# Performance work log

Measured on AMD Instinct MI355X. Metric: run time of the kernel, lower is better.

The kernel has to match this reference:

```python
import jax, jax.numpy as jnp
import numpy as np
import math

B, T, C = 2, 2048, 2048
N_HEAD = 16
N_KV = 4
GROUP = N_HEAD // N_KV
HS = C // N_HEAD
WINDOW = 1024
SINK = 4


def setup_inputs() -> dict:
    key = jax.random.key(0)
    ks = jax.random.split(key, 5)
    s = 1.0 / math.sqrt(C)
    return {
        "x": jax.random.normal(ks[0], (B, T, C), dtype=jnp.float32),
        "Wq": jax.random.normal(ks[1], (C, C), dtype=jnp.float32) * s,
        "Wk": jax.random.normal(ks[2], (N_KV * HS, C), dtype=jnp.float32) * s,
        "Wv": jax.random.normal(ks[3], (N_KV * HS, C), dtype=jnp.float32) * s,
        "Wo": jax.random.normal(ks[4], (C, C), dtype=jnp.float32) * s,
    }


def _sliding_window_sink_mask(t):
    i = jnp.arange(t)[:, None]  # query index
    j = jnp.arange(t)[None, :]  # key index
    causal = j <= i
    band = j >= i - (WINDOW - 1)
    mask = causal & band
    mask = mask | (j < SINK)          # sink columns always visible
    mask = mask & ((i >= SINK) | causal)  # sink rows stay strictly causal
    return mask  # (T, T) bool


def reference(x, Wq, Wk, Wv, Wo):
    b, t, c = x.shape
    q = (x @ Wq.T).reshape(b, t, N_HEAD, HS).transpose(0, 2, 1, 3)
    # group q heads by kv head: (B, n_kv, group, T, hs)
    q = q.reshape(b, N_KV, GROUP, t, HS)
    k = (x @ Wk.T).reshape(b, t, N_KV, HS).transpose(0, 2, 1, 3)  # (B, n_kv, T, hs)
    v = (x @ Wv.T).reshape(b, t, N_KV, HS).transpose(0, 2, 1, 3)
    scale = 1.0 / math.sqrt(HS)
    # scores over full TxT (faithful to original, K/V expansion done via broadcast)
    att = jnp.einsum('bkgqd,bkjd->bkgqj', q, k) * scale
    mask = _sliding_window_sink_mask(t)  # (T, T)
    att = jnp.where(mask[None, None, None, :, :], att, -jnp.inf)
    att = jax.nn.softmax(att, axis=-1)
    y = jnp.einsum('bkgqj,bkjd->bkgqd', att, v)
    y = y.reshape(b, N_HEAD, t, HS).transpose(0, 2, 1, 3).reshape(b, t, c)
    return y @ Wo.T
```

## Files before the change

### kernel.cpp

```cpp
#include <hip/hip_runtime.h>


#define T_SEQ 2048
#define NKV   4
#define HS    128
#define CDIM  2048
#define QKVN  3072
#define WIN   1024
#define SINKN 4
#define PSTR  68

typedef __bf16 bf16x8 __attribute__((ext_vector_type(8)));
typedef float  f32x4  __attribute__((ext_vector_type(4)));

#define MFMA16(A, B, C) __builtin_amdgcn_mfma_f32_16x16x32_bf16(A, B, C, 0, 0, 0)
#define EXP2(x) __builtin_amdgcn_exp2f(x)

__device__ inline unsigned short f2bu(float f) {
  unsigned int u = __float_as_uint(f);
  u += 0x7fffu + ((u >> 16) & 1u);
  return (unsigned short)(u >> 16);
}
__device__ inline unsigned int pkhi(float f0, float f1) {
  return __builtin_amdgcn_perm(__float_as_uint(f1), __float_as_uint(f0),
                               0x07060302u);
}
__device__ inline __bf16 us2b(unsigned short u) {
  union { unsigned short u; __bf16 b; } t; t.u = u; return t.b;
}
__device__ inline f32x4 fzero4() { f32x4 z = {0.f, 0.f, 0.f, 0.f}; return z; }

__device__ __forceinline__ void glds16(const void* g, const void* lds_uniform) {
  typedef __attribute__((address_space(1))) void gv;
  typedef __attribute__((address_space(3))) void lv;
  __builtin_amdgcn_global_load_lds((gv*)(unsigned long long)g,
                                   (lv*)(unsigned int)(unsigned long long)lds_uniform,
                                   16, 0, 0);
}

#define SZ_X  8388608
#define SZ_WQ 4194304
#define SZ_WK 1048576
#define OFF_WQ (SZ_X)
#define OFF_WK (SZ_X + SZ_WQ)
#define OFF_WV (OFF_WK + SZ_WK)
#define OFF_WO (OFF_WV + SZ_WK)
#define SZ_ALL (OFF_WO + SZ_WQ)

__global__ __launch_bounds__(256) void f2b_all(const float* __restrict__ x,
                                               const float* __restrict__ wq,
                                               const float* __restrict__ wk,
                                               const float* __restrict__ wv,
                                               const float* __restrict__ wo,
                                               unsigned short* __restrict__ out,
                                               float qs) {
  int i = (blockIdx.x * 256 + threadIdx.x) * 4;
  const float* src; int off; float sc = 1.0f;
  if (i < OFF_WQ)      { src = x;  off = 0; }
  else if (i < OFF_WK) { src = wq; off = OFF_WQ; sc = qs; }
  else if (i < OFF_WV) { src = wk; off = OFF_WK; }
  else if (i < OFF_WO) { src = wv; off = OFF_WV; }
  else                 { src = wo; off = OFF_WO; }
  float4 v = *reinterpret_cast<const float4*>(src + (i - off));
  ushort4 o;
  o.x = f2bu(v.x * sc); o.y = f2bu(v.y * sc);
  o.z = f2bu(v.z * sc); o.w = f2bu(v.w * sc);
  *reinterpret_cast<ushort4*>(out + i) = o;
}

__device__ inline void storeC(unsigned short* p, float v) { *p = f2bu(v); }
__device__ inline void storeC(float* p, float v) { *p = v; }

template <typename OutT>
__global__ __launch_bounds__(512, 2) void gemm256(const unsigned short* __restrict__ A,
                                                  const unsigned short* __restrict__ B,
                                                  OutT* __restrict__ C,
                                                  int M, int N, int K) {
  __shared__ __align__(16) unsigned short As[2][16384];
  __shared__ __align__(16) unsigned short Bs[2][16384];
  const int tid  = threadIdx.x;
  const int wave = tid >> 6, lane = tid & 63;
  const int quad = lane >> 4, l16 = lane & 15;
  const int wmi  = wave >> 2, wni = wave & 3;
  const int sx   = ((l16 >> 3) & 1) << 5;

  const int tmn  = M >> 8;
  const int qq   = gridDim.x >> 3;
  const int swzb = (blockIdx.x & 7) * qq + (blockIdx.x >> 3);
  const int tm   = (swzb % tmn) << 8;
  const int tn   = (swzb / tmn) << 8;

  const int logl = (lane * 16) ^ (((lane >> 5) & 1) << 5);
  const int srow = logl >> 6;
  const int scol = (logl & 63) >> 1;
  const int NT   = K >> 6;

  auto issueA = [&](int tt, int ch) {
    glds16(&A[(size_t)(tm + (ch & 15) * 16 + srow) * K + (tt << 6) + (ch >> 4) * 32 + scol],
           (const char*)As + ((tt & 1) << 15) + ch * 1024);
  };
  auto issueB = [&](int tt, int ch) {
    glds16(&B[(size_t)(tn + (ch & 15) * 16 + srow) * K + (tt << 6) + (ch >> 4) * 32 + scol],
           (const char*)Bs + ((tt & 1) << 15) + ch * 1024);
  };

  f32x4 acc[8][4];
#pragma unroll
  for (int i = 0; i < 8; ++i)
#pragma unroll
    for (int j = 0; j < 4; ++j) acc[i][j] = fzero4();

  issueB(0, wave); issueB(0, 8 + wave); issueB(0, 16 + wave); issueB(0, 24 + wave);
  issueA(0, wave); issueA(0, 16 + wave); issueA(0, 8 + wave); issueA(0, 24 + wave);
  if (NT > 1) {
    issueB(1, wave); issueB(1, 8 + wave);
    asm volatile("s_waitcnt vmcnt(2)" ::: "memory");
  } else {
    asm volatile("s_waitcnt vmcnt(0)" ::: "memory");
  }
  __builtin_amdgcn_s_barrier();

#pragma unroll 2
  for (int t = 0; t < NT; ++t) {
    const char* Asc = (const char*)As + ((t & 1) << 15);
    const char* Bsc = (const char*)Bs + ((t & 1) << 15);
    const bool h1 = (t + 1 < NT), h2 = (t + 2 < NT);
    bf16x8 aq[4], bq[4];

#pragma unroll
    for (int g = 0; g < 4; ++g)
      bq[g] = *reinterpret_cast<const bf16x8*>(
          Bsc + (((wni * 64 + g * 16 + l16) << 6) + ((quad * 16) ^ sx)));
#pragma unroll
    for (int f = 0; f < 4; ++f)
      aq[f] = *reinterpret_cast<const bf16x8*>(
          Asc + (((wmi * 128 + f * 16 + l16) << 6) + ((quad * 16) ^ sx)));
    if (h1) { issueB(t + 1, 16 + wave); issueB(t + 1, 24 + wave); }
    __builtin_amdgcn_s_barrier();
    asm volatile("s_waitcnt lgkmcnt(0)" ::: "memory");
    __builtin_amdgcn_s_setprio(1);
#pragma unroll
    for (int f = 0; f < 4; ++f)
#pragma unroll
      for (int g = 0; g < 4; ++g) acc[f][g] = MFMA16(aq[f], bq[g], acc[f][g]);
    __builtin_amdgcn_s_setprio(0);
    __builtin_amdgcn_s_barrier();

#pragma unroll
    for (int f = 0; f < 4; ++f)
      aq[f] = *reinterpret_cast<const bf16x8*>(
          Asc + (((wmi * 128 + 64 + f * 16 + l16) << 6) + ((quad * 16) ^ sx)));
    if (h1) { issueA(t + 1, wave); issueA(t + 1, 16 + wave); }
    __builtin_amdgcn_s_barrier();
    asm volatile("s_waitcnt lgkmcnt(0)" ::: "memory");
    __builtin_amdgcn_s_setprio(1);
#pragma unroll
    for (int f = 0; f < 4; ++f)
#pragma unroll
      for (int g = 0; g < 4; ++g) acc[4 + f][g] = MFMA16(aq[f], bq[g], acc[4 + f][g]);
    __builtin_amdgcn_s_setprio(0);
    __builtin_amdgcn_s_barrier();

#pragma unroll
    for (int g = 0; g < 4; ++g)
      bq[g] = *reinterpret_cast<const bf16x8*>(
          Bsc + (16384 + ((wni * 64 + g * 16 + l16) << 6) + ((quad * 16) ^ sx)));
#pragma unroll
    for (int f = 0; f < 4; ++f)
      aq[f] = *reinterpret_cast<const bf16x8*>(
          Asc + (16384 + ((wmi * 128 + f * 16 + l16) << 6) + ((quad * 16) ^ sx)));
    if (h1) { issueA(t + 1, 8 + wave); issueA(t + 1, 24 + wave); }
    __builtin_amdgcn_s_barrier();
    asm volatile("s_waitcnt lgkmcnt(0)" ::: "memory");
    __builtin_amdgcn_s_setprio(1);
#pragma unroll
    for (int f = 0; f < 4; ++f)
#pragma unroll
      for (int g = 0; g < 4; ++g) acc[f][g] = MFMA16(aq[f], bq[g], acc[f][g]);
    __builtin_amdgcn_s_setprio(0);
    __builtin_amdgcn_s_barrier();

#pragma unroll
    for (int f = 0; f < 4; ++f)
      aq[f] = *reinterpret_cast<const bf16x8*>(
          Asc + (16384 + ((wmi * 128 + 64 + f * 16 + l16) << 6) + ((quad * 16) ^ sx)));
    if (h2) { issueB(t + 2, wave); issueB(t + 2, 8 + wave); }
    __builtin_amdgcn_s_barrier();
    asm volatile("s_waitcnt lgkmcnt(0)" ::: "memory");
    __builtin_amdgcn_s_setprio(1);
#pragma unroll
    for (int f = 0; f < 4; ++f)
#pragma unroll
      for (int g = 0; g < 4; ++g) acc[4 + f][g] = MFMA16(aq[f], bq[g], acc[4 + f][g]);
    __builtin_amdgcn_s_setprio(0);
    if (h2) asm volatile("s_waitcnt vmcnt(2)" ::: "memory");
    else    asm volatile("s_waitcnt vmcnt(0)" ::: "memory");
    __builtin_amdgcn_s_barrier();
  }

#pragma unroll
  for (int fi = 0; fi < 8; ++fi)
#pragma unroll
    for (int g = 0; g < 4; ++g)
#pragma unroll
      for (int r = 0; r < 4; ++r) {
        const int row = tm + wmi * 128 + fi * 16 + quad * 4 + r;
        const int col = tn + wni * 64 + g * 16 + l16;
        storeC(&C[(size_t)row * N + col], acc[fi][g][r]);
      }
}

template <typename OutT>
__global__ __launch_bounds__(512, 2) void gemm_bn128(const unsigned short* __restrict__ A,
                                                     const unsigned short* __restrict__ B,
                                                     OutT* __restrict__ C,
                                                     int M, int N, int K) {
  __shared__ __align__(16) unsigned short As[2][16384];
  __shared__ __align__(16) unsigned short Bs[2][8192];
  const int tid  = threadIdx.x;
  const int wave = tid >> 6, lane = tid & 63;
  const int quad = lane >> 4, l16 = lane & 15;
  const int wmi  = wave >> 1, wni = wave & 1;
  const int sx   = ((l16 >> 3) & 1) << 5;

  const int tmn  = M >> 8;
  const int qq   = gridDim.x >> 3;
  const int swzb = (blockIdx.x & 7) * qq + (blockIdx.x >> 3);
  const int tm   = (swzb % tmn) << 8;
  const int tn   = (swzb / tmn) << 7;

  const int logl = (lane * 16) ^ (((lane >> 5) & 1) << 5);
  const int srow = logl >> 6;
  const int scol = (logl & 63) >> 1;
  const int NT   = K >> 6;

  auto issueA = [&](int tt, int ch) {
    glds16(&A[(size_t)(tm + (ch & 15) * 16 + srow) * K + (tt << 6) + (ch >> 4) * 32 + scol],
           (const char*)As + ((tt & 1) << 15) + ch * 1024);
  };
  auto issueB = [&](int tt, int ch) {
    glds16(&B[(size_t)(tn + (ch & 7) * 16 + srow) * K + (tt << 6) + (ch >> 3) * 32 + scol],
           (const char*)Bs + ((tt & 1) << 14) + ch * 1024);
  };

  f32x4 acc[4][4];
#pragma unroll
  for (int i = 0; i < 4; ++i)
#pragma unroll
    for (int j = 0; j < 4; ++j) acc[i][j] = fzero4();

  issueB(0, wave);     issueA(0, wave);      issueA(0, 8 + wave);
  issueB(0, 8 + wave); issueA(0, 16 + wave); issueA(0, 24 + wave);
  if (NT > 1) {
    issueB(1, wave); issueA(1, wave); issueA(1, 8 + wave);
    asm volatile("s_waitcnt vmcnt(6)" ::: "memory");
  } else {
    asm volatile("s_waitcnt vmcnt(3)" ::: "memory");
  }
  __builtin_amdgcn_s_barrier();

  for (int t = 0; t < NT; ++t) {
    const char* Asc = (const char*)As + ((t & 1) << 15);
    const char* Bsc = (const char*)Bs + ((t & 1) << 14);
    const bool h1 = (t + 1 < NT), h2 = (t + 2 < NT);
    bf16x8 aq[4], bq[4];

#pragma unroll
    for (int g = 0; g < 4; ++g)
      bq[g] = *reinterpret_cast<const bf16x8*>(
          Bsc + (((wni * 64 + g * 16 + l16) << 6) + ((quad * 16) ^ sx)));
#pragma unroll
    for (int f = 0; f < 4; ++f)
      aq[f] = *reinterpret_cast<const bf16x8*>(
          Asc + (((wmi * 64 + f * 16 + l16) << 6) + ((quad * 16) ^ sx)));
    if (h1) {
      issueB(t + 1, 8 + wave); issueA(t + 1, 16 + wave); issueA(t + 1, 24 + wave);
    }
    __builtin_amdgcn_s_barrier();
    asm volatile("s_waitcnt lgkmcnt(0)" ::: "memory");
    __builtin_amdgcn_s_setprio(1);
#pragma unroll
    for (int f = 0; f < 4; ++f)
#pragma unroll
      for (int g = 0; g < 4; ++g) acc[f][g] = MFMA16(aq[f], bq[g], acc[f][g]);
    __builtin_amdgcn_s_setprio(0);
    if (h1) asm volatile("s_waitcnt vmcnt(6)" ::: "memory");
    else    asm volatile("s_waitcnt vmcnt(0)" ::: "memory");
    __builtin_amdgcn_s_barrier();

#pragma unroll
    for (int g = 0; g < 4; ++g)
      bq[g] = *reinterpret_cast<const bf16x8*>(
          Bsc + (8192 + ((wni * 64 + g * 16 + l16) << 6) + ((quad * 16) ^ sx)));
#pragma unroll
    for (int f = 0; f < 4; ++f)
      aq[f] = *reinterpret_cast<const bf16x8*>(
          Asc + (16384 + ((wmi * 64 + f * 16 + l16) << 6) + ((quad * 16) ^ sx)));
    if (h2) {
      issueB(t + 2, wave); issueA(t + 2, wave); issueA(t + 2, 8 + wave);
    }
    __builtin_amdgcn_s_barrier();
    asm volatile("s_waitcnt lgkmcnt(0)" ::: "memory");
    __builtin_amdgcn_s_setprio(1);
#pragma unroll
    for (int f = 0; f < 4; ++f)
#pragma unroll
      for (int g = 0; g < 4; ++g) acc[f][g] = MFMA16(aq[f], bq[g], acc[f][g]);
    __builtin_amdgcn_s_setprio(0);
    if (h2)      asm volatile("s_waitcnt vmcnt(6)" ::: "memory");
    else if (h1) asm volatile("s_waitcnt vmcnt(3)" ::: "memory");
    else         asm volatile("s_waitcnt vmcnt(0)" ::: "memory");
    __builtin_amdgcn_s_barrier();
  }

#pragma unroll
  for (int fi = 0; fi < 4; ++fi)
#pragma unroll
    for (int g = 0; g < 4; ++g)
#pragma unroll
      for (int r = 0; r < 4; ++r) {
        const int row = tm + wmi * 64 + fi * 16 + quad * 4 + r;
        const int col = tn + wni * 64 + g * 16 + l16;
        storeC(&C[(size_t)row * N + col], acc[fi][g][r]);
      }
}

__global__ __launch_bounds__(256) void kvpack(const unsigned short* __restrict__ QKV,
                                              unsigned short* __restrict__ Kp,
                                              unsigned short* __restrict__ Vp) {
  const int tid  = threadIdx.x;
  const int kt64 = blockIdx.x;
  const int bk   = blockIdx.y;
  const int b = bk >> 2, kvh = bk & 3;
  const int kt = kt64 * 64;
  const int bT = b * T_SEQ;
  const int dq = tid & 15;

  unsigned short* kdst = &Kp[(size_t)(bk * 32 + kt64) * 8192];
#pragma unroll
  for (int it = 0; it < 4; ++it) {
    int key = it * 16 + (tid >> 4);
    float4 v = *reinterpret_cast<const float4*>(
        &QKV[(size_t)(bT + kt + key) * QKVN + 2048 + kvh * HS + dq * 8]);
    int c = dq >> 2, quad = dq & 3, nt = key & 3, l16s = key >> 2;
    *reinterpret_cast<float4*>(
        &kdst[((size_t)((c * 4 + nt) * 64 + quad * 16 + l16s)) * 8]) = v;
  }

#pragma unroll
  for (int it = 0; it < 4; ++it) {
    int key = it * 16 + (tid >> 4);
    float4 v = *reinterpret_cast<const float4*>(
        &QKV[(size_t)(bT + kt + key) * QKVN + 2560 + kvh * HS + dq * 8]);
    const unsigned short* pv = reinterpret_cast<const unsigned short*>(&v);
    int kt32 = kt64 * 2 + (key >> 5);
    int quad = (key & 31) >> 3, j = key & 7;
    unsigned short* vdst = &Vp[(size_t)(bk * 64 + kt32) * 4096];
#pragma unroll
    for (int j2 = 0; j2 < 8; ++j2) {
      int d = dq * 8 + j2, dt = d >> 4, l16v = d & 15;
      vdst[((size_t)(dt * 64 + quad * 16 + l16v)) * 8 + j] = pv[j2];
    }
  }
}

__global__ __launch_bounds__(256) void attn_kernel(const unsigned short* __restrict__ QKV,
                                                   const unsigned short* __restrict__ Kp,
                                                   const unsigned short* __restrict__ Vp,
                                                   unsigned short* __restrict__ Y) {
  __shared__ __align__(16) unsigned short KVs[16384];
  __shared__ __align__(16) unsigned short Ps[4 * 32 * PSTR];
  unsigned short* Ks = KVs;
  unsigned short* Vs = KVs + 8192;

  const int tid  = threadIdx.x;
  const int wave = tid >> 6, lane = tid & 63;
  const int quad = lane >> 4, l16 = lane & 15;
  const int qt0 = (int)(gridDim.x - 1 - blockIdx.x) * 32;
  const int kvh = blockIdx.y, b = blockIdx.z;
  const int h   = kvh * 4 + wave;
  const int bk  = b * NKV + kvh;
  const int bT  = b * T_SEQ;
  unsigned short* Pw = &Ps[wave * 32 * PSTR];

  bf16x8 qa[2][4];
#pragma unroll
  for (int mt = 0; mt < 2; ++mt)
#pragma unroll
    for (int c = 0; c < 4; ++c)
      qa[mt][c] = *reinterpret_cast<const bf16x8*>(
          &QKV[(size_t)(bT + qt0 + mt * 16 + l16) * QKVN + h * HS + c * 32 + quad * 8]);

  bf16x8 ones;
#pragma unroll
  for (int j = 0; j < 8; ++j) ones[j] = us2b(0x3F80);

  f32x4 o[2][9];
#pragma unroll
  for (int mt = 0; mt < 2; ++mt)
#pragma unroll
    for (int dt = 0; dt < 9; ++dt) o[mt][dt] = fzero4();

  const int start = (qt0 >= 1024) ? ((qt0 - 1023) & ~63) : 0;
  const int sink  = (start > 0) ? 1 : 0;
  const int nch   = ((qt0 + 32 - start + 63) >> 6) + sink;

  for (int ci = 0; ci < nch; ++ci) {
    const bool is_sink = (sink && ci == 0);
    const int  kt  = is_sink ? 0 : start + (ci - sink) * 64;
    const int  rem = qt0 + 32 - kt;
    const int  kcmax = is_sink ? 1 : (rem >= 64 ? 2 : ((rem + 31) >> 5));
    const bool full  = !is_sink && (kt + 63 <= qt0) && (kt >= qt0 - 992);

    __syncthreads();
    {
      const unsigned short* kg = &Kp[(size_t)(bk * 32 + (kt >> 6)) * 8192 + lane * 8];
      const unsigned short* vg = &Vp[(size_t)(bk * 64 + (kt >> 5)) * 4096 + lane * 8];
#pragma unroll
      for (int i = 0; i < 4; ++i) {
        int part = wave * 4 + i;
        glds16(kg + part * 512, &Ks[part * 512]);
        glds16(vg + part * 512, &Vs[part * 512]);
      }
    }
    __syncthreads();

    f32x4 s[2][4];
#pragma unroll
    for (int nt = 0; nt < 4; ++nt) { s[0][nt] = fzero4(); s[1][nt] = fzero4(); }
#pragma unroll
    for (int c = 0; c < 4; ++c) {
#pragma unroll
      for (int nt = 0; nt < 4; ++nt) {
        bf16x8 kf = *reinterpret_cast<const bf16x8*>(&Ks[(c * 4 + nt) * 512 + lane * 8]);
        s[0][nt] = MFMA16(qa[0][c], kf, s[0][nt]);
        s[1][nt] = MFMA16(qa[1][c], kf, s[1][nt]);
      }
    }

    if (full) {
#pragma unroll
      for (int mt = 0; mt < 2; ++mt)
#pragma unroll
        for (int r = 0; r < 4; ++r) {
          const int row = mt * 16 + quad * 4 + r;
          uint2 pk;
          pk.x = pkhi(EXP2(s[mt][0][r]), EXP2(s[mt][1][r]));
          pk.y = pkhi(EXP2(s[mt][2][r]), EXP2(s[mt][3][r]));
          *reinterpret_cast<uint2*>(&Pw[row * PSTR + l16 * 4]) = pk;
        }
    } else {
#pragma unroll
      for (int mt = 0; mt < 2; ++mt)
#pragma unroll
        for (int r = 0; r < 4; ++r) {
          const int row = mt * 16 + quad * 4 + r;
          const int qi  = qt0 + row;
          float p[4];
#pragma unroll
          for (int nt = 0; nt < 4; ++nt) {
            int kj = kt + l16 * 4 + nt;
            bool ok = ((kj <= qi) && (kj + (WIN - 1) >= qi)) ||
                      ((kj < SINKN) && (qi >= SINKN));
            p[nt] = ok ? EXP2(s[mt][nt][r]) : 0.f;
          }
          uint2 pk;
          pk.x = pkhi(p[0], p[1]);
          pk.y = pkhi(p[2], p[3]);
          *reinterpret_cast<uint2*>(&Pw[row * PSTR + l16 * 4]) = pk;
        }
    }
    asm volatile("s_waitcnt lgkmcnt(0)" ::: "memory");

#pragma unroll
    for (int kc = 0; kc < 2; ++kc)
      if (kc < kcmax) {
#pragma unroll
        for (int mt = 0; mt < 2; ++mt) {
          bf16x8 pf = *reinterpret_cast<const bf16x8*>(
              &Pw[(mt * 16 + l16) * PSTR + kc * 32 + quad * 8]);
#pragma unroll
          for (int dt = 0; dt < 8; ++dt) {
            bf16x8 vf = *reinterpret_cast<const bf16x8*>(
                &Vs[kc * 4096 + dt * 512 + lane * 8]);
            o[mt][dt] = MFMA16(pf, vf, o[mt][dt]);
          }
          o[mt][8] = MFMA16(pf, ones, o[mt][8]);
        }
      }
  }

  __syncthreads();
  unsigned short* Yst = KVs;
#pragma unroll
  for (int mt = 0; mt < 2; ++mt) {
    float inv[4];
#pragma unroll
    for (int r = 0; r < 4; ++r) inv[r] = __builtin_amdgcn_rcpf(o[mt][8][r]);
#pragma unroll
    for (int dt = 0; dt < 8; ++dt)
#pragma unroll
      for (int r = 0; r < 4; ++r)
        Yst[(mt * 16 + quad * 4 + r) * 512 + wave * 128 + dt * 16 + l16] =
            f2bu(o[mt][dt][r] * inv[r]);
  }
  __syncthreads();
#pragma unroll
  for (int it = 0; it < 8; ++it) {
    int idx = it * 256 + tid;
    int row = idx >> 6, col = (idx & 63) * 8;
    *reinterpret_cast<uint4*>(
        &Y[(size_t)(bT + qt0 + row) * CDIM + kvh * 512 + col]) =
        *reinterpret_cast<const uint4*>(&Yst[row * 512 + col]);
  }
}

extern "C" void kernel_launch(void* const* d_in, const int* in_sizes, int n_in,
                              void* d_out, int out_size, void* d_ws, size_t ws_size,
                              hipStream_t stream) {
  const float* x  = (const float*)d_in[0];
  const float* Wq = (const float*)d_in[1];
  const float* Wk = (const float*)d_in[2];
  const float* Wv = (const float*)d_in[3];
  const float* Wo = (const float*)d_in[4];
  float* out = (float*)d_out;

  unsigned short* base = (unsigned short*)d_ws;
  unsigned short* xb   = base;
  unsigned short* wqb  = xb + OFF_WQ;
  unsigned short* wob  = xb + OFF_WO;
  unsigned short* QKVb = xb + SZ_ALL;
  unsigned short* Kpb  = wqb;
  unsigned short* Vpb  = wqb + 2097152;
  unsigned short* Yb   = xb;

  const float qscale = 0.08838834764831845f * 1.4426950408889634f;
  f2b_all<<<SZ_ALL / 1024, 256, 0, stream>>>(x, Wq, Wk, Wv, Wo, xb, qscale);

  gemm256<unsigned short><<<192, 512, 0, stream>>>(xb, wqb, QKVb, 4096, QKVN, 2048);

  kvpack<<<dim3(32, 8), 256, 0, stream>>>(QKVb, Kpb, Vpb);

  attn_kernel<<<dim3(64, 4, 2), 256, 0, stream>>>(QKVb, Kpb, Vpb, Yb);

  gemm_bn128<float><<<256, 512, 0, stream>>>(Yb, wob, out, 4096, 2048, 2048);
}
```

Baseline: 273.4 us.

## Retile QKV projection GEMM to 256x192 tiles for 256-block grid

Replaces the 256x256-tile QKV GEMM with a 256x192-tile variant, so the grid grows from 192 to 256 blocks and better fills the MI355X's 256 CUs. Waves are rearranged as a 4x2 grid, each computing 64x96 outputs. The K-loop is rewritten as two half-steps per 64-wide k-tile with a new prefetch and vmcnt wait schedule. In exchange it loses some data reuse per tile and adds risk in the hand-tuned wait counts.

```diff
diff --git a/kernel.cpp b/kernel.cpp
--- a/kernel.cpp
+++ b/kernel.cpp
@@ -72,23 +72,23 @@
 __device__ inline void storeC(float* p, float v) { *p = v; }
 
 template <typename OutT>
-__global__ __launch_bounds__(512, 2) void gemm256(const unsigned short* __restrict__ A,
-                                                  const unsigned short* __restrict__ B,
-                                                  OutT* __restrict__ C,
-                                                  int M, int N, int K) {
+__global__ __launch_bounds__(512, 2) void gemm_bn192(const unsigned short* __restrict__ A,
+                                                     const unsigned short* __restrict__ B,
+                                                     OutT* __restrict__ C,
+                                                     int M, int N, int K) {
   __shared__ __align__(16) unsigned short As[2][16384];
-  __shared__ __align__(16) unsigned short Bs[2][16384];
+  __shared__ __align__(16) unsigned short Bs[2][12288];
   const int tid  = threadIdx.x;
   const int wave = tid >> 6, lane = tid & 63;
   const int quad = lane >> 4, l16 = lane & 15;
-  const int wmi  = wave >> 2, wni = wave & 3;
+  const int wmi  = wave >> 1, wni = wave & 1;
   const int sx   = ((l16 >> 3) & 1) << 5;
 
   const int tmn  = M >> 8;
   const int qq   = gridDim.x >> 3;
   const int swzb = (blockIdx.x & 7) * qq + (blockIdx.x >> 3);
   const int tm   = (swzb % tmn) << 8;
-  const int tn   = (swzb / tmn) << 8;
+  const int tn   = (swzb / tmn) * 192;
 
   const int logl = (lane * 16) ^ (((lane >> 5) & 1) << 5);
   const int srow = logl >> 6;
@@ -99,113 +99,93 @@
     glds16(&A[(size_t)(tm + (ch & 15) * 16 + srow) * K + (tt << 6) + (ch >> 4) * 32 + scol],
            (const char*)As + ((tt & 1) << 15) + ch * 1024);
   };
-  auto issueB = [&](int tt, int ch) {
-    glds16(&B[(size_t)(tn + (ch & 15) * 16 + srow) * K + (tt << 6) + (ch >> 4) * 32 + scol],
-           (const char*)Bs + ((tt & 1) << 15) + ch * 1024);
+  auto issueB = [&](int tt, int kh, int rb) {
+    glds16(&B[(size_t)(tn + rb * 16 + srow) * K + (tt << 6) + kh * 32 + scol],
+           (const char*)Bs + (tt & 1) * 24576 + (kh * 12 + rb) * 1024);
   };
-
-  f32x4 acc[8][4];
-#pragma unroll
-  for (int i = 0; i < 8; ++i)
-#pragma unroll
-    for (int j = 0; j < 4; ++j) acc[i][j] = fzero4();
-
-  issueB(0, wave); issueB(0, 8 + wave); issueB(0, 16 + wave); issueB(0, 24 + wave);
-  issueA(0, wave); issueA(0, 16 + wave); issueA(0, 8 + wave); issueA(0, 24 + wave);
+  const int g3kh = (wave >= 4) ? 1 : 0;
+  const int g3rb = (wave >= 4) ? (wave - 4) : (8 + wave);
+
+  f32x4 acc[4][6];
+#pragma unroll
+  for (int i = 0; i < 4; ++i)
+#pragma unroll
+    for (int j = 0; j < 6; ++j) acc[i][j] = fzero4();
+
+  issueA(0, wave); issueA(0, 8 + wave); issueB(0, 0, wave);
+  issueA(0, 16 + wave); issueA(0, 24 + wave); issueB(0, 1, 4 + wave);
+  issueB(0, g3kh, g3rb);
   if (NT > 1) {
-    issueB(1, wave); issueB(1, 8 + wave);
-    asm volatile("s_waitcnt vmcnt(2)" ::: "memory");
+    issueA(1, wave); issueA(1, 8 + wave); issueB(1, 0, wave);
+    asm volatile("s_waitcnt vmcnt(3)" ::: "memory");
   } else {
     asm volatile("s_waitcnt vmcnt(0)" ::: "memory");
   }
   __builtin_amdgcn_s_barrier();
 
-#pragma unroll 2
   for (int t = 0; t < NT; ++t) {
     const char* Asc = (const char*)As + ((t & 1) << 15);
-    const char* Bsc = (const char*)Bs + ((t & 1) << 15);
+    const char* Bsc = (const char*)Bs + (t & 1) * 24576;
     const bool h1 = (t + 1 < NT), h2 = (t + 2 < NT);
-    bf16x8 aq[4], bq[4];
-
-#pragma unroll
-    for (int g = 0; g < 4; ++g)
+    bf16x8 aq[4], bq[6];
+
+#pragma unroll
+    for (int g = 0; g < 6; ++g)
       bq[g] = *reinterpret_cast<const bf16x8*>(
-          Bsc + (((wni * 64 + g * 16 + l16) << 6) + ((quad * 16) ^ sx)));
+          Bsc + (((wni * 96 + g * 16 + l16) << 6) + ((quad * 16) ^ sx)));
 #pragma unroll
     for (int f = 0; f < 4; ++f)
       aq[f] = *reinterpret_cast<const bf16x8*>(
-          Asc + (((wmi * 128 + f * 16 + l16) << 6) + ((quad * 16) ^ sx)));
-    if (h1) { issueB(t + 1, 16 + wave); issueB(t + 1, 24 + wave); }
+          Asc + (((wmi * 64 + f * 16 + l16) << 6) + ((quad * 16) ^ sx)));
+    if (h1) {
+      issueA(t + 1, 16 + wave); issueA(t + 1, 24 + wave);
+      issueB(t + 1, 1, 4 + wave); issueB(t + 1, g3kh, g3rb);
+    }
     __builtin_amdgcn_s_barrier();
     asm volatile("s_waitcnt lgkmcnt(0)" ::: "memory");
     __builtin_amdgcn_s_setprio(1);
 #pragma unroll
     for (int f = 0; f < 4; ++f)
 #pragma unroll
-      for (int g = 0; g < 4; ++g) acc[f][g] = MFMA16(aq[f], bq[g], acc[f][g]);
+      for (int g = 0; g < 6; ++g) acc[f][g] = MFMA16(aq[f], bq[g], acc[f][g]);
     __builtin_amdgcn_s_setprio(0);
-    __builtin_amdgcn_s_barrier();
-
+    if (h1) asm volatile("s_waitcnt vmcnt(7)" ::: "memory");
+    else    asm volatile("s_waitcnt vmcnt(0)" ::: "memory");
+    __builtin_amdgcn_s_barrier();
+
+#pragma unroll
+    for (int g = 0; g < 6; ++g)
+      bq[g] = *reinterpret_cast<const bf16x8*>(
+          Bsc + (12288 + ((wni * 96 + g * 16 + l16) << 6) + ((quad * 16) ^ sx)));
 #pragma unroll
     for (int f = 0; f < 4; ++f)
       aq[f] = *reinterpret_cast<const bf16x8*>(
-          Asc + (((wmi * 128 + 64 + f * 16 + l16) << 6) + ((quad * 16) ^ sx)));
-    if (h1) { issueA(t + 1, wave); issueA(t + 1, 16 + wave); }
+          Asc + (16384 + ((wmi * 64 + f * 16 + l16) << 6) + ((quad * 16) ^ sx)));
+    if (h2) {
+      issueA(t + 2, wave); issueA(t + 2, 8 + wave); issueB(t + 2, 0, wave);
+    }
     __builtin_amdgcn_s_barrier();
     asm volatile("s_waitcnt lgkmcnt(0)" ::: "memory");
     __builtin_amdgcn_s_setprio(1);
 #pragma unroll
     for (int f = 0; f < 4; ++f)
 #pragma unroll
-      for (int g = 0; g < 4; ++g) acc[4 + f][g] = MFMA16(aq[f], bq[g], acc[4 + f][g]);
+      for (int g = 0; g < 6; ++g) acc[f][g] = MFMA16(aq[f], bq[g], acc[f][g]);
     __builtin_amdgcn_s_setprio(0);
-    __builtin_amdgcn_s_barrier();
-
-#pragma unroll
-    for (int g = 0; g < 4; ++g)
-      bq[g] = *reinterpret_cast<const bf16x8*>(
-          Bsc + (16384 + ((wni * 64 + g * 16 + l16) << 6) + ((quad * 16) ^ sx)));
-#pragma unroll
-    for (int f = 0; f < 4; ++f)
-      aq[f] = *reinterpret_cast<const bf16x8*>(
-          Asc + (16384 + ((wmi * 128 + f * 16 + l16) << 6) + ((quad * 16) ^ sx)));
-    if (h1) { issueA(t + 1, 8 + wave); issueA(t + 1, 24 + wave); }
-    __builtin_amdgcn_s_barrier();
-    asm volatile("s_waitcnt lgkmcnt(0)" ::: "memory");
-    __builtin_amdgcn_s_setprio(1);
-#pragma unroll
-    for (int f = 0; f < 4; ++f)
-#pragma unroll
-      for (int g = 0; g < 4; ++g) acc[f][g] = MFMA16(aq[f], bq[g], acc[f][g]);
-    __builtin_amdgcn_s_setprio(0);
-    __builtin_amdgcn_s_barrier();
-
-#pragma unroll
-    for (int f = 0; f < 4; ++f)
-      aq[f] = *reinterpret_cast<const bf16x8*>(
-          Asc + (16384 + ((wmi * 128 + 64 + f * 16 + l16) << 6) + ((quad * 16) ^ sx)));
-    if (h2) { issueB(t + 2, wave); issueB(t + 2, 8 + wave); }
-    __builtin_amdgcn_s_barrier();
-    asm volatile("s_waitcnt lgkmcnt(0)" ::: "memory");
-    __builtin_amdgcn_s_setprio(1);
-#pragma unroll
-    for (int f = 0; f < 4; ++f)
-#pragma unroll
-      for (int g = 0; g < 4; ++g) acc[4 + f][g] = MFMA16(aq[f], bq[g], acc[4 + f][g]);
-    __builtin_amdgcn_s_setprio(0);
-    if (h2) asm volatile("s_waitcnt vmcnt(2)" ::: "memory");
-    else    asm volatile("s_waitcnt vmcnt(0)" ::: "memory");
-    __builtin_amdgcn_s_barrier();
-  }
-
-#pragma unroll
-  for (int fi = 0; fi < 8; ++fi)
-#pragma unroll
-    for (int g = 0; g < 4; ++g)
+    if (h2)      asm volatile("s_waitcnt vmcnt(7)" ::: "memory");
+    else if (h1) asm volatile("s_waitcnt vmcnt(4)" ::: "memory");
+    else         asm volatile("s_waitcnt vmcnt(0)" ::: "memory");
+    __builtin_amdgcn_s_barrier();
+  }
+
+#pragma unroll
+  for (int fi = 0; fi < 4; ++fi)
+#pragma unroll
+    for (int g = 0; g < 6; ++g)
 #pragma unroll
       for (int r = 0; r < 4; ++r) {
-        const int row = tm + wmi * 128 + fi * 16 + quad * 4 + r;
-        const int col = tn + wni * 64 + g * 16 + l16;
+        const int row = tm + wmi * 64 + fi * 16 + quad * 4 + r;
+        const int col = tn + wni * 96 + g * 16 + l16;
         storeC(&C[(size_t)row * N + col], acc[fi][g][r]);
       }
 }
@@ -537,7 +517,7 @@
   const float qscale = 0.08838834764831845f * 1.4426950408889634f;
   f2b_all<<<SZ_ALL / 1024, 256, 0, stream>>>(x, Wq, Wk, Wv, Wo, xb, qscale);
 
-  gemm256<unsigned short><<<192, 512, 0, stream>>>(xb, wqb, QKVb, 4096, QKVN, 2048);
+  gemm_bn192<unsigned short><<<256, 512, 0, stream>>>(xb, wqb, QKVb, 4096, QKVN, 2048);
 
   kvpack<<<dim3(32, 8), 256, 0, stream>>>(QKVb, Kpb, Vpb);
 
```

Measured after the change: 263.6 us. 3.6% less time.
